# Kernel tuning notes

Hardware: AMD Instinct MI355X
Metric: run time of the kernel (lower is better)

Reference implementation:

```python
import jax, jax.numpy as jnp
import numpy as np

N_NODES = 50000
N_EDGES = 800000
N_GRAPHS = 128
ORIG_FEA = 92
NBR_FEA = 41
H = 64
N_CONV = 3
BN_EPS = 1e-5


def setup_inputs() -> dict:
    key = jax.random.key(0)
    ks = jax.random.split(key, 16)
    x = jax.random.normal(ks[0], (N_NODES, ORIG_FEA), dtype=jnp.float32)
    edge_attr = jax.random.normal(ks[1], (N_EDGES, NBR_FEA), dtype=jnp.float32)
    edge_index = jax.random.randint(ks[2], (2, N_EDGES), 0, N_NODES)
    batch = jnp.sort(jax.random.randint(ks[3], (N_NODES,), 0, N_GRAPHS))
    s_emb1 = 1.0 / np.sqrt(ORIG_FEA)
    s_emb2 = 1.0 / np.sqrt(NBR_FEA)
    s_conv = 1.0 / np.sqrt(3 * H)
    s_h = 1.0 / np.sqrt(H)
    return {
        "x": x,
        "edge_attr": edge_attr,
        "edge_index": edge_index,
        "batch": batch,
        "W_emb1": jax.random.uniform(ks[4], (ORIG_FEA, H), jnp.float32, -s_emb1, s_emb1),
        "b_emb1": jnp.zeros((H,), jnp.float32),
        "W_emb2": jax.random.uniform(ks[5], (NBR_FEA, H), jnp.float32, -s_emb2, s_emb2),
        "b_emb2": jnp.zeros((H,), jnp.float32),
        "Wf": jax.random.uniform(ks[6], (N_CONV, 3 * H, H), jnp.float32, -s_conv, s_conv),
        "bf": jnp.zeros((N_CONV, H), jnp.float32),
        "Ws": jax.random.uniform(ks[7], (N_CONV, 3 * H, H), jnp.float32, -s_conv, s_conv),
        "bs": jnp.zeros((N_CONV, H), jnp.float32),
        "gamma": jnp.ones((N_CONV, H), jnp.float32),
        "beta": jnp.zeros((N_CONV, H), jnp.float32),
        "W1": jax.random.uniform(ks[8], (H, H), jnp.float32, -s_h, s_h),
        "b1": jnp.zeros((H,), jnp.float32),
        "W2": jax.random.uniform(ks[9], (H, H), jnp.float32, -s_h, s_h),
        "b2": jnp.zeros((H,), jnp.float32),
        "Wo": jax.random.uniform(ks[10], (H, 1), jnp.float32, -s_h, s_h),
        "bo": jnp.zeros((1,), jnp.float32),
    }


def _batch_norm(h, g, b):
    # training-mode BatchNorm1d: biased batch statistics
    mu = jnp.mean(h, axis=0)
    var = jnp.var(h, axis=0)
    return (h - mu) * jax.lax.rsqrt(var + BN_EPS) * g + b


def reference(x, edge_attr, edge_index, batch, W_emb1, b_emb1, W_emb2, b_emb2,
              Wf, bf, Ws, bs, gamma, beta, W1, b1, W2, b2, Wo, bo):
    src = edge_index[0]  # x_j (source)
    dst = edge_index[1]  # x_i (target, aggregation index)
    h = x @ W_emb1 + b_emb1              # [N, H]
    e = edge_attr @ W_emb2 + b_emb2      # [E, H]
    for a in range(N_CONV):
        # CGConv: z_ij = [x_i, x_j, e_ij]; msg = sigmoid(lin_f(z)) * softplus(lin_s(z))
        z = jnp.concatenate([h[dst], h[src], e], axis=1)       # [E, 3H]
        msg = jax.nn.sigmoid(z @ Wf[a] + bf[a]) * jax.nn.softplus(z @ Ws[a] + bs[a])
        h = h + jax.ops.segment_sum(msg, dst, num_segments=N_NODES)
        h = _batch_norm(h, gamma[a], beta[a])
        if a != N_CONV - 1:
            h = jax.nn.relu(h)
        # dropout ratio is 0 -> no-op
    # JK='last' -> node representation is final h; mean pooling per graph
    sums = jax.ops.segment_sum(h, batch, num_segments=N_GRAPHS)              # [G, H]
    cnts = jax.ops.segment_sum(jnp.ones((N_NODES,), h.dtype), batch, num_segments=N_GRAPHS)
    y = sums / jnp.maximum(cnts, 1.0)[:, None]
    y = jax.nn.softplus(y @ W1 + b1)
    y = jax.nn.softplus(y @ W2 + b2)
    y = (y @ Wo + bo).squeeze(-1)  # [G]
    return y
```

## Files before the change

kernel.cpp:

```cpp
#include <hip/hip_runtime.h>
#include <hip/hip_bf16.h>
#include <hip/hip_fp16.h>
#include <math.h>

#define N_NODES 50000
#define N_EDGES 800000
#define N_GRAPHS 128
#define ORIG_FEA 92
#define NBR_FEA 41
#define H 64
#define N_CONV 3
#define BN_EPS 1e-5f
#define KP 48

typedef _Float16 h8 __attribute__((ext_vector_type(8)));
typedef float f32x4 __attribute__((ext_vector_type(4)));

__device__ __forceinline__ float sigmoidf_(float x) {
    return __fdividef(1.f, 1.f + __expf(-x));
}
__device__ __forceinline__ float softplusf_(float x) {
    return fmaxf(x, 0.f) + __logf(1.f + __expf(-fabsf(x)));
}

__global__ __launch_bounds__(256) void fold_kernel(
    const float* __restrict__ W_emb2, const float* __restrict__ b_emb2,
    const float* __restrict__ Wf, const float* __restrict__ bf,
    const float* __restrict__ Ws, const float* __restrict__ bs,
    _Float16* __restrict__ W2frag, float* __restrict__ cfs) {
    int a = blockIdx.x >> 1, gate = blockIdx.x & 1;
    const float* W = (gate ? Ws : Wf) + a * 192 * H + 128 * H;
    const float* bias = (gate ? bs : bf) + a * H;
    _Float16* out = W2frag + a * 128 * 64;
    float* cout = cfs + a * 128;
    for (int idx = threadIdx.x; idx < 64 * 64; idx += blockDim.x) {
        int j = idx >> 6, k = idx & 63;
        float acc = 0.f;
        if (k < NBR_FEA)
            for (int m = 0; m < H; ++m) acc += W_emb2[k * H + m] * W[m * H + j];
        int frag = (gate * 4 + (j >> 4)) * 2 + (k >> 5);
        int lane = (((k & 31) >> 3) << 4) + (j & 15);
        out[(frag * 64 + lane) * 8 + (k & 7)] = (_Float16)acc;
    }
    for (int j = threadIdx.x; j < H; j += blockDim.x) {
        float acc = bias[j];
        for (int m = 0; m < H; ++m) acc += b_emb2[m] * W[m * H + j];
        cout[(j & 15) * 8 + gate * 4 + (j >> 4)] = acc;
    }
}

__global__ __launch_bounds__(256) void embed_kernel(
    const float* __restrict__ x, const float* __restrict__ W,
    const float* __restrict__ b, float* __restrict__ state) {
    __shared__ float lw[ORIG_FEA * H];
    for (int i = threadIdx.x; i < ORIG_FEA * H; i += blockDim.x) lw[i] = W[i];
    __syncthreads();
    int lane = threadIdx.x & 63;
    int wid = (blockIdx.x * blockDim.x + threadIdx.x) >> 6;
    int nw = (gridDim.x * blockDim.x) >> 6;
    for (int n = wid; n < N_NODES; n += nw) {
        int nu = __builtin_amdgcn_readfirstlane(n);
        const float* xr = x + (size_t)nu * ORIG_FEA;
        float acc = b[lane];
#pragma unroll
        for (int k = 0; k < ORIG_FEA; ++k) acc += xr[k] * lw[k * H + lane];
        state[(size_t)nu * H + lane] = acc;
    }
}

__global__ __launch_bounds__(256) void hist_kernel(
    const int* __restrict__ ei, int* __restrict__ deg) {
    int e = blockIdx.x * blockDim.x + threadIdx.x;
    if (e < N_EDGES) atomicAdd(&deg[ei[N_EDGES + e]], 1);
}

__global__ __launch_bounds__(256) void scan_kernel(
    const int* __restrict__ deg, int* __restrict__ off, int* __restrict__ cur) {
    __shared__ int part[256];
    const int CHN = (N_NODES + 255) / 256;
    int t = threadIdx.x;
    int lo = t * CHN, hi = min(lo + CHN, N_NODES);
    int s = 0;
    for (int i = lo; i < hi; ++i) s += deg[i];
    part[t] = s;
    __syncthreads();
    for (int o = 1; o < 256; o <<= 1) {
        int v = (t >= o) ? part[t - o] : 0;
        __syncthreads();
        part[t] += v;
        __syncthreads();
    }
    int run = (t == 0) ? 0 : part[t - 1];
    for (int i = lo; i < hi; ++i) {
        off[i] = run;
        cur[i] = run;
        run += deg[i];
    }
    if (t == 255) off[N_NODES] = run;
}

__global__ __launch_bounds__(256) void scatter_kernel(
    const int* __restrict__ ei, int* __restrict__ cur, int* __restrict__ pos,
    int* __restrict__ src_s) {
    int e = blockIdx.x * blockDim.x + threadIdx.x;
    if (e < N_EDGES) {
        int d = ei[N_EDGES + e];
        int p = atomicAdd(&cur[d], 1);
        pos[e] = p;
        src_s[p] = ei[e];
    }
}

__global__ __launch_bounds__(256) void pack_ea_kernel(
    const int* __restrict__ pos, const float* __restrict__ ea,
    _Float16* __restrict__ ea_p) {
    int lane = threadIdx.x & 63;
    int wid = (blockIdx.x * blockDim.x + threadIdx.x) >> 6;
    int nw = (gridDim.x * blockDim.x) >> 6;
    for (int e = wid; e < N_EDGES; e += nw) {
        int eu = __builtin_amdgcn_readfirstlane(e);
        int p = __builtin_amdgcn_readfirstlane(pos[eu]);
        unsigned dw = 0;
        if (lane < 21) {
            const float* er = ea + (size_t)eu * NBR_FEA;
            float v0 = er[2 * lane];
            float v1 = (2 * lane + 1 < NBR_FEA) ? er[2 * lane + 1] : 0.f;
            union { _Float16 h[2]; unsigned u; } cv;
            cv.h[0] = (_Float16)v0;
            cv.h[1] = (_Float16)v1;
            dw = cv.u;
        }
        if (lane < KP / 2)
            *(unsigned*)(ea_p + (size_t)p * KP + 2 * lane) = dw;
    }
}

__global__ __launch_bounds__(256) void node_proj_bn_kernel(
    const float* __restrict__ state, const float* __restrict__ stats,
    const float* __restrict__ gamma, const float* __restrict__ beta,
    const float* __restrict__ Wf, const float* __restrict__ Ws,
    float* __restrict__ NPi, float* __restrict__ NPj, int mode) {
    __shared__ float lw[4 * H * H];
    __shared__ float slot[4][H];
    for (int i = threadIdx.x; i < H * H; i += blockDim.x) {
        lw[i] = Wf[i];
        lw[H * H + i] = Wf[H * H + i];
        lw[2 * H * H + i] = Ws[i];
        lw[3 * H * H + i] = Ws[H * H + i];
    }
    int lane = threadIdx.x & 63;
    int wl = threadIdx.x >> 6;
    int gbase = (lane & 15) * 8 + (lane >> 4);
    float A = 1.f, B = 0.f;
    if (mode) {
        const float inv_n = 1.f / (float)N_NODES;
        float mu = stats[lane] * inv_n;
        float var = stats[H + lane] * inv_n - mu * mu;
        float inv = rsqrtf(var + BN_EPS);
        A = inv * gamma[lane];
        B = beta[lane] - mu * A;
    }
    __syncthreads();
    int wid = (blockIdx.x * blockDim.x + threadIdx.x) >> 6;
    int nw = (gridDim.x * blockDim.x) >> 6;
    for (int n = wid; n < N_NODES; n += nw) {
        float z = state[(size_t)n * H + lane];
        float hn = mode ? fmaxf(z * A + B, 0.f) : z;
        slot[wl][lane] = hn;
        float pf = 0.f, qf = 0.f, ps = 0.f, qs = 0.f;
#pragma unroll
        for (int k = 0; k < H; ++k) {
            float s = slot[wl][k];
            pf += s * lw[k * H + lane];
            qf += s * lw[H * H + k * H + lane];
            ps += s * lw[2 * H * H + k * H + lane];
            qs += s * lw[3 * H * H + k * H + lane];
        }
        NPi[(size_t)n * 128 + gbase] = pf;
        NPi[(size_t)n * 128 + gbase + 4] = ps;
        NPj[(size_t)n * 128 + gbase] = qf;
        NPj[(size_t)n * 128 + gbase + 4] = qs;
    }
}

__global__ __launch_bounds__(256) void edge_mfma_kernel(
    const int* __restrict__ off, const int* __restrict__ src_s,
    const _Float16* __restrict__ ea_p,
    const float* __restrict__ NPi, const float* __restrict__ NPj,
    const _Float16* __restrict__ W2frag, const float* __restrict__ cfs,
    const float* __restrict__ stats_prev, const float* __restrict__ gamma,
    const float* __restrict__ beta, float* __restrict__ state,
    float* __restrict__ stats_out, int mode) {
    int lane = threadIdx.x & 63;
    int m15 = lane & 15, g = lane >> 4;
    h8 bfr[8][2];
#pragma unroll
    for (int nt = 0; nt < 8; ++nt)
#pragma unroll
        for (int ks = 0; ks < 2; ++ks) {
            union { uint4 u; h8 h; } cv;
            cv.u = *(const uint4*)(W2frag + (size_t)(((nt * 2 + ks) * 64) + lane) * 8);
            bfr[nt][ks] = cv.h;
        }
    f32x4 cflo = *(const f32x4*)(cfs + m15 * 8);
    f32x4 cfhi = *(const f32x4*)(cfs + m15 * 8 + 4);
    float A = 1.f, B = 0.f;
    if (mode) {
        const float inv_n = 1.f / (float)N_NODES;
        float mu = stats_prev[lane] * inv_n;
        float var = stats_prev[H + lane] * inv_n - mu * mu;
        float inv = rsqrtf(var + BN_EPS);
        A = inv * gamma[lane];
        B = beta[lane] - mu * A;
    }
    float s = 0.f, s2 = 0.f;
    int wid = (blockIdx.x * blockDim.x + threadIdx.x) >> 6;
    int nw = (gridDim.x * blockDim.x) >> 6;
    for (int n = wid; n < N_NODES; n += nw) {
        int nu = __builtin_amdgcn_readfirstlane(n);
        float z = state[(size_t)nu * H + lane];
        float acc = mode ? fmaxf(z * A + B, 0.f) : z;
        f32x4 nplo = *(const f32x4*)(NPi + (size_t)nu * 128 + m15 * 8);
        f32x4 nphi = *(const f32x4*)(NPi + (size_t)nu * 128 + m15 * 8 + 4);
        f32x4 bfv = cflo + nplo;
        f32x4 bsv = cfhi + nphi;
        int e0 = __builtin_amdgcn_readfirstlane(off[nu]);
        int e1 = __builtin_amdgcn_readfirstlane(off[nu + 1]);
        if (e0 >= e1) {
            state[(size_t)nu * H + lane] = acc;
            s += acc;
            s2 += acc * acc;
            continue;
        }
        h8 afr0, afr1;
        {
            int arow = min(e0 + m15, e1 - 1);
            const _Float16* rowp = ea_p + (size_t)arow * KP;
            union { uint4 u; h8 h; } cv0, cv1;
            cv0.u = *(const uint4*)(rowp + g * 8);
            afr0 = cv0.h;
            const _Float16* p1 = rowp + ((g < 2) ? (32 + g * 8) : 0);
            uint4 r1 = *(const uint4*)p1;
            if (g >= 2) { r1.x = 0u; r1.y = 0u; r1.z = 0u; r1.w = 0u; }
            cv1.u = r1;
            afr1 = cv1.h;
        }
        for (int e = e0; e < e1; e += 16) {
            int cnt = e1 - e;
            f32x4 c[8];
#pragma unroll
            for (int nt = 0; nt < 8; ++nt) c[nt] = (f32x4)(0.f);
#pragma unroll
            for (int nt = 0; nt < 8; ++nt)
                c[nt] = __builtin_amdgcn_mfma_f32_16x16x32_f16(afr0, bfr[nt][0],
                                                               c[nt], 0, 0, 0);
#pragma unroll
            for (int nt = 0; nt < 8; ++nt)
                c[nt] = __builtin_amdgcn_mfma_f32_16x16x32_f16(afr1, bfr[nt][1],
                                                               c[nt], 0, 0, 0);
            int en = e + 16;
            if (en < e1) {
                int arow = min(en + m15, e1 - 1);
                const _Float16* rowp = ea_p + (size_t)arow * KP;
                union { uint4 u; h8 h; } cv0, cv1;
                cv0.u = *(const uint4*)(rowp + g * 8);
                afr0 = cv0.h;
                const _Float16* p1 = rowp + ((g < 2) ? (32 + g * 8) : 0);
                uint4 r1 = *(const uint4*)p1;
                if (g >= 2) { r1.x = 0u; r1.y = 0u; r1.z = 0u; r1.w = 0u; }
                cv1.u = r1;
                afr1 = cv1.h;
            }
            f32x4 ql[4], qh[4];
            float mul[4];
#pragma unroll
            for (int r = 0; r < 4; ++r) {
                int rr = 4 * g + r;
                int ee = e + ((rr < cnt) ? rr : (cnt - 1));
                int sv = src_s[ee];
                const float* qp = NPj + (size_t)sv * 128 + m15 * 8;
                ql[r] = *(const f32x4*)qp;
                qh[r] = *(const f32x4*)(qp + 4);
                mul[r] = (rr < cnt) ? 1.f : 0.f;
            }
            float ts0 = 0.f, ts1 = 0.f, ts2 = 0.f, ts3 = 0.f;
#pragma unroll
            for (int r = 0; r < 4; ++r) {
                {
                    float af = c[0][r] + bfv[0] + ql[r][0];
                    float as = c[4][r] + bsv[0] + qh[r][0];
                    ts0 += mul[r] * sigmoidf_(af) * softplusf_(as);
                }
                {
                    float af = c[1][r] + bfv[1] + ql[r][1];
                    float as = c[5][r] + bsv[1] + qh[r][1];
                    ts1 += mul[r] * sigmoidf_(af) * softplusf_(as);
                }
                {
                    float af = c[2][r] + bfv[2] + ql[r][2];
                    float as = c[6][r] + bsv[2] + qh[r][2];
                    ts2 += mul[r] * sigmoidf_(af) * softplusf_(as);
                }
                {
                    float af = c[3][r] + bfv[3] + ql[r][3];
                    float as = c[7][r] + bsv[3] + qh[r][3];
                    ts3 += mul[r] * sigmoidf_(af) * softplusf_(as);
                }
            }
            ts0 += __shfl_xor(ts0, 16, 64); ts0 += __shfl_xor(ts0, 32, 64);
            ts1 += __shfl_xor(ts1, 16, 64); ts1 += __shfl_xor(ts1, 32, 64);
            ts2 += __shfl_xor(ts2, 16, 64); ts2 += __shfl_xor(ts2, 32, 64);
            ts3 += __shfl_xor(ts3, 16, 64); ts3 += __shfl_xor(ts3, 32, 64);
            float v = (g & 2) ? ((g & 1) ? ts3 : ts2) : ((g & 1) ? ts1 : ts0);
            acc += v;
        }
        state[(size_t)nu * H + lane] = acc;
        s += acc;
        s2 += acc * acc;
    }
    atomicAdd(&stats_out[lane], s);
    atomicAdd(&stats_out[H + lane], s2);
}

__global__ __launch_bounds__(256) void pool_bn_kernel(
    const float* __restrict__ state, const float* __restrict__ stats,
    const float* __restrict__ gamma, const float* __restrict__ beta,
    const int* __restrict__ batch, float* __restrict__ gsum,
    float* __restrict__ gcnt) {
    int lane = threadIdx.x & 63;
    const float inv_n = 1.f / (float)N_NODES;
    float mu = stats[lane] * inv_n;
    float var = stats[H + lane] * inv_n - mu * mu;
    float inv = rsqrtf(var + BN_EPS);
    float A = inv * gamma[lane];
    float B = beta[lane] - mu * A;
    int wid = (blockIdx.x * blockDim.x + threadIdx.x) >> 6;
    int nw = (gridDim.x * blockDim.x) >> 6;
    int per = (N_NODES + nw - 1) / nw;
    int lo = wid * per, hi = min(lo + per, N_NODES);
    if (lo >= hi) return;
    int gcur = __builtin_amdgcn_readfirstlane(batch[lo]);
    float accv = 0.f, cntv = 0.f;
    for (int n = lo; n < hi; ++n) {
        int gn = __builtin_amdgcn_readfirstlane(batch[n]);
        if (gn != gcur) {
            atomicAdd(&gsum[(size_t)gcur * H + lane], accv);
            if (lane == 0) atomicAdd(&gcnt[gcur], cntv);
            gcur = gn;
            accv = 0.f;
            cntv = 0.f;
        }
        accv += state[(size_t)n * H + lane] * A + B;
        cntv += 1.f;
    }
    atomicAdd(&gsum[(size_t)gcur * H + lane], accv);
    if (lane == 0) atomicAdd(&gcnt[gcur], cntv);
}

__global__ __launch_bounds__(64) void mlp_kernel(
    const float* __restrict__ gsum, const float* __restrict__ gcnt,
    const float* __restrict__ W1, const float* __restrict__ b1,
    const float* __restrict__ W2, const float* __restrict__ b2,
    const float* __restrict__ Wo, const float* __restrict__ bo,
    float* __restrict__ out) {
    int g = blockIdx.x;
    int lane = threadIdx.x;
    __shared__ float y[H];
    float cnt = fmaxf(gcnt[g], 1.f);
    y[lane] = gsum[(size_t)g * H + lane] / cnt;
    __syncthreads();
    float acc = b1[lane];
#pragma unroll
    for (int k = 0; k < H; ++k) acc += y[k] * W1[k * H + lane];
    float y1 = softplusf_(acc);
    __syncthreads();
    y[lane] = y1;
    __syncthreads();
    acc = b2[lane];
#pragma unroll
    for (int k = 0; k < H; ++k) acc += y[k] * W2[k * H + lane];
    float y2 = softplusf_(acc);
    float t = y2 * Wo[lane];
#pragma unroll
    for (int o = 32; o > 0; o >>= 1) t += __shfl_down(t, o, 64);
    if (lane == 0) out[g] = t + bo[0];
}

extern "C" void kernel_launch(void* const* d_in, const int* in_sizes, int n_in,
                              void* d_out, int out_size, void* d_ws, size_t ws_size,
                              hipStream_t stream) {
    const float* x = (const float*)d_in[0];
    const float* ea = (const float*)d_in[1];
    const int* ei = (const int*)d_in[2];
    const int* batch = (const int*)d_in[3];
    const float* W_emb1 = (const float*)d_in[4];
    const float* b_emb1 = (const float*)d_in[5];
    const float* W_emb2 = (const float*)d_in[6];
    const float* b_emb2 = (const float*)d_in[7];
    const float* Wf = (const float*)d_in[8];
    const float* bf = (const float*)d_in[9];
    const float* Ws = (const float*)d_in[10];
    const float* bs = (const float*)d_in[11];
    const float* gamma = (const float*)d_in[12];
    const float* beta = (const float*)d_in[13];
    const float* W1 = (const float*)d_in[14];
    const float* b1 = (const float*)d_in[15];
    const float* W2 = (const float*)d_in[16];
    const float* b2 = (const float*)d_in[17];
    const float* Wo = (const float*)d_in[18];
    const float* bo = (const float*)d_in[19];
    float* out = (float*)d_out;

    float* w = (float*)d_ws;
    float* stats = w;
    float* gsum = stats + 3 * 2 * H;
    float* gcnt = gsum + N_GRAPHS * H;
    int* deg = (int*)(gcnt + N_GRAPHS);
    const size_t zero_elems = 3 * 2 * H + N_GRAPHS * H + N_GRAPHS + N_NODES;
    _Float16* ea_p = (_Float16*)(w + zero_elems);
    int* off = (int*)(ea_p + (size_t)(N_EDGES + 8) * KP);
    int* cur = off + 50004;
    int* pos = cur + N_NODES;
    int* src_s = pos + N_EDGES;
    _Float16* W2frag = (_Float16*)(src_s + N_EDGES);
    float* cfs = (float*)(W2frag + 3 * 128 * 64);
    float* state = cfs + 3 * 128;
    float* NPi = state + (size_t)N_NODES * H;
    float* NPj = NPi + (size_t)N_NODES * 128;

    hipMemsetAsync(w, 0, zero_elems * sizeof(float), stream);

    fold_kernel<<<6, 256, 0, stream>>>(W_emb2, b_emb2, Wf, bf, Ws, bs, W2frag, cfs);
    embed_kernel<<<512, 256, 0, stream>>>(x, W_emb1, b_emb1, state);
    hist_kernel<<<(N_EDGES + 255) / 256, 256, 0, stream>>>(ei, deg);
    scan_kernel<<<1, 256, 0, stream>>>(deg, off, cur);
    scatter_kernel<<<(N_EDGES + 255) / 256, 256, 0, stream>>>(ei, cur, pos, src_s);
    pack_ea_kernel<<<2048, 256, 0, stream>>>(pos, ea, ea_p);

    for (int a = 0; a < N_CONV; ++a) {
        const float* sp = a > 0 ? stats + (a - 1) * 2 * H : stats;
        const float* gp = a > 0 ? gamma + (a - 1) * H : gamma;
        const float* bp = a > 0 ? beta + (a - 1) * H : beta;
        int mode = a > 0 ? 1 : 0;
        node_proj_bn_kernel<<<512, 256, 0, stream>>>(
            state, sp, gp, bp, Wf + a * 192 * H, Ws + a * 192 * H, NPi, NPj, mode);
        edge_mfma_kernel<<<2048, 256, 0, stream>>>(
            off, src_s, ea_p, NPi, NPj, W2frag + a * 128 * 64, cfs + a * 128,
            sp, gp, bp, state, stats + a * 2 * H, mode);
    }

    pool_bn_kernel<<<784, 256, 0, stream>>>(state, stats + 2 * 2 * H,
                                            gamma + 2 * H, beta + 2 * H,
                                            batch, gsum, gcnt);
    mlp_kernel<<<128, 64, 0, stream>>>(gsum, gcnt, W1, b1, W2, b2, Wo, bo, out);
}
```

Measured before the change: 1.248 ms.

## Use MFMA for node projections, store source projections in fp16, move edge weights to LDS

The scalar FMA node projection is replaced by an fp16 MFMA kernel that uses pre-packed concatenated Wf/Ws fragments, prepared by a new prep kernel. The source-side projection NPj is stored as fp16, which halves the bytes of the per-edge random gather. The edge kernel now reads its weight fragments from shared memory instead of holding them in registers, to cut register pressure and raise occupancy. It also drops the software prefetch of the next edge tile and changes the grid size. Risks are fp16 rounding error on the projected features and extra LDS traffic in the edge loop.

```diff
diff --git a/kernel.cpp b/kernel.cpp
--- a/kernel.cpp
+++ b/kernel.cpp
@@ -49,6 +49,23 @@
     }
 }
 
+__global__ __launch_bounds__(256) void prep_wcat_kernel(
+    const float* __restrict__ Wf, const float* __restrict__ Ws,
+    _Float16* __restrict__ Wcat_frag) {
+    int a = blockIdx.x;
+    _Float16* out = Wcat_frag + a * 64 * 256;
+    for (int idx = threadIdx.x; idx < 64 * 256; idx += blockDim.x) {
+        int k = idx >> 8, col = idx & 255;
+        int proj = col >> 6, j = col & 63;
+        int gate = proj & 1, ij = proj >> 1;
+        const float* W = (gate ? Ws : Wf) + a * 192 * H;
+        float v = W[(ij * 64 + k) * H + j];
+        int nt = col >> 4;
+        int lane = (((k & 31) >> 3) << 4) + (j & 15);
+        out[((nt * 2 + (k >> 5)) * 64 + lane) * 8 + (k & 7)] = (_Float16)v;
+    }
+}
+
 __global__ __launch_bounds__(256) void embed_kernel(
     const float* __restrict__ x, const float* __restrict__ W,
     const float* __restrict__ b, float* __restrict__ state) {
@@ -135,73 +152,108 @@
     }
 }
 
-__global__ __launch_bounds__(256) void node_proj_bn_kernel(
+__global__ __launch_bounds__(256, 4) void node_proj_mfma_kernel(
     const float* __restrict__ state, const float* __restrict__ stats,
     const float* __restrict__ gamma, const float* __restrict__ beta,
-    const float* __restrict__ Wf, const float* __restrict__ Ws,
-    float* __restrict__ NPi, float* __restrict__ NPj, int mode) {
-    __shared__ float lw[4 * H * H];
-    __shared__ float slot[4][H];
-    for (int i = threadIdx.x; i < H * H; i += blockDim.x) {
-        lw[i] = Wf[i];
-        lw[H * H + i] = Wf[H * H + i];
-        lw[2 * H * H + i] = Ws[i];
-        lw[3 * H * H + i] = Ws[H * H + i];
-    }
+    const _Float16* __restrict__ Wcat_frag,
+    float* __restrict__ NPi, _Float16* __restrict__ NPj, int mode) {
+    __shared__ __align__(16) _Float16 lB[32 * 64 * 8];
+    for (int i = threadIdx.x * 8; i < 32 * 64 * 8; i += blockDim.x * 8)
+        *(uint4*)(lB + i) = *(const uint4*)(Wcat_frag + i);
+    __syncthreads();
     int lane = threadIdx.x & 63;
-    int wl = threadIdx.x >> 6;
-    int gbase = (lane & 15) * 8 + (lane >> 4);
-    float A = 1.f, B = 0.f;
-    if (mode) {
-        const float inv_n = 1.f / (float)N_NODES;
-        float mu = stats[lane] * inv_n;
-        float var = stats[H + lane] * inv_n - mu * mu;
-        float inv = rsqrtf(var + BN_EPS);
-        A = inv * gamma[lane];
-        B = beta[lane] - mu * A;
-    }
-    __syncthreads();
+    int m15 = lane & 15, g = lane >> 4;
+    f32x4 Ac[2][2], Bc[2][2];
+#pragma unroll
+    for (int ks = 0; ks < 2; ++ks)
+#pragma unroll
+        for (int hlf = 0; hlf < 2; ++hlf) {
+            int k0 = ks * 32 + g * 8 + hlf * 4;
+            if (mode) {
+                const float inv_n = 1.f / (float)N_NODES;
+                f32x4 sm = *(const f32x4*)(stats + k0);
+                f32x4 sq = *(const f32x4*)(stats + H + k0);
+                f32x4 gm = *(const f32x4*)(gamma + k0);
+                f32x4 bt = *(const f32x4*)(beta + k0);
+#pragma unroll
+                for (int i = 0; i < 4; ++i) {
+                    float mu = sm[i] * inv_n;
+                    float var = sq[i] * inv_n - mu * mu;
+                    float inv = rsqrtf(var + BN_EPS);
+                    Ac[ks][hlf][i] = inv * gm[i];
+                    Bc[ks][hlf][i] = bt[i] - mu * inv * gm[i];
+                }
+            } else {
+                Ac[ks][hlf] = (f32x4)(1.f);
+                Bc[ks][hlf] = (f32x4)(0.f);
+            }
+        }
     int wid = (blockIdx.x * blockDim.x + threadIdx.x) >> 6;
     int nw = (gridDim.x * blockDim.x) >> 6;
-    for (int n = wid; n < N_NODES; n += nw) {
-        float z = state[(size_t)n * H + lane];
-        float hn = mode ? fmaxf(z * A + B, 0.f) : z;
-        slot[wl][lane] = hn;
-        float pf = 0.f, qf = 0.f, ps = 0.f, qs = 0.f;
-#pragma unroll
-        for (int k = 0; k < H; ++k) {
-            float s = slot[wl][k];
-            pf += s * lw[k * H + lane];
-            qf += s * lw[H * H + k * H + lane];
-            ps += s * lw[2 * H * H + k * H + lane];
-            qs += s * lw[3 * H * H + k * H + lane];
-        }
-        NPi[(size_t)n * 128 + gbase] = pf;
-        NPi[(size_t)n * 128 + gbase + 4] = ps;
-        NPj[(size_t)n * 128 + gbase] = qf;
-        NPj[(size_t)n * 128 + gbase + 4] = qs;
-    }
-}
-
-__global__ __launch_bounds__(256) void edge_mfma_kernel(
+    for (int t = wid; t < 3125; t += nw) {
+        int node = t * 16 + m15;
+        const float* sr = state + (size_t)node * H;
+        h8 afr[2];
+#pragma unroll
+        for (int ks = 0; ks < 2; ++ks) {
+            f32x4 z0 = *(const f32x4*)(sr + ks * 32 + g * 8);
+            f32x4 z1 = *(const f32x4*)(sr + ks * 32 + g * 8 + 4);
+            h8 a;
+#pragma unroll
+            for (int i = 0; i < 4; ++i) {
+                float v0 = z0[i] * Ac[ks][0][i] + Bc[ks][0][i];
+                float v1 = z1[i] * Ac[ks][1][i] + Bc[ks][1][i];
+                if (mode) { v0 = fmaxf(v0, 0.f); v1 = fmaxf(v1, 0.f); }
+                a[i] = (_Float16)v0;
+                a[4 + i] = (_Float16)v1;
+            }
+            afr[ks] = a;
+        }
+        f32x4 c[16];
+#pragma unroll
+        for (int nt = 0; nt < 16; ++nt) c[nt] = (f32x4)(0.f);
+#pragma unroll
+        for (int ks = 0; ks < 2; ++ks)
+#pragma unroll
+            for (int nt = 0; nt < 16; ++nt) {
+                h8 b = *(const h8*)(lB + ((size_t)(nt * 2 + ks) * 64 + lane) * 8);
+                c[nt] = __builtin_amdgcn_mfma_f32_16x16x32_f16(afr[ks], b, c[nt],
+                                                               0, 0, 0);
+            }
+#pragma unroll
+        for (int r = 0; r < 4; ++r) {
+            int nr = t * 16 + 4 * g + r;
+            f32x4 lo, hi;
+            h8 qj;
+#pragma unroll
+            for (int fq = 0; fq < 4; ++fq) {
+                lo[fq] = c[fq][r];
+                hi[fq] = c[4 + fq][r];
+                qj[fq] = (_Float16)c[8 + fq][r];
+                qj[4 + fq] = (_Float16)c[12 + fq][r];
+            }
+            float* pi = NPi + (size_t)nr * 128 + m15 * 8;
+            *(f32x4*)pi = lo;
+            *(f32x4*)(pi + 4) = hi;
+            *(h8*)(NPj + (size_t)nr * 128 + m15 * 8) = qj;
+        }
+    }
+}
+
+__global__ __launch_bounds__(256, 5) void edge_mfma_kernel(
     const int* __restrict__ off, const int* __restrict__ src_s,
     const _Float16* __restrict__ ea_p,
-    const float* __restrict__ NPi, const float* __restrict__ NPj,
+    const float* __restrict__ NPi, const _Float16* __restrict__ NPj,
     const _Float16* __restrict__ W2frag, const float* __restrict__ cfs,
     const float* __restrict__ stats_prev, const float* __restrict__ gamma,
     const float* __restrict__ beta, float* __restrict__ state,
     float* __restrict__ stats_out, int mode) {
+    __shared__ __align__(16) _Float16 lB[128 * 64];
+    for (int i = threadIdx.x * 8; i < 128 * 64; i += blockDim.x * 8)
+        *(uint4*)(lB + i) = *(const uint4*)(W2frag + i);
+    __syncthreads();
     int lane = threadIdx.x & 63;
     int m15 = lane & 15, g = lane >> 4;
-    h8 bfr[8][2];
-#pragma unroll
-    for (int nt = 0; nt < 8; ++nt)
-#pragma unroll
-        for (int ks = 0; ks < 2; ++ks) {
-            union { uint4 u; h8 h; } cv;
-            cv.u = *(const uint4*)(W2frag + (size_t)(((nt * 2 + ks) * 64) + lane) * 8);
-            bfr[nt][ks] = cv.h;
-        }
     f32x4 cflo = *(const f32x4*)(cfs + m15 * 8);
     f32x4 cfhi = *(const f32x4*)(cfs + m15 * 8 + 4);
     float A = 1.f, B = 0.f;
@@ -226,42 +278,12 @@
         f32x4 bsv = cfhi + nphi;
         int e0 = __builtin_amdgcn_readfirstlane(off[nu]);
         int e1 = __builtin_amdgcn_readfirstlane(off[nu + 1]);
-        if (e0 >= e1) {
-            state[(size_t)nu * H + lane] = acc;
-            s += acc;
-            s2 += acc * acc;
-            continue;
-        }
-        h8 afr0, afr1;
-        {
-            int arow = min(e0 + m15, e1 - 1);
-            const _Float16* rowp = ea_p + (size_t)arow * KP;
-            union { uint4 u; h8 h; } cv0, cv1;
-            cv0.u = *(const uint4*)(rowp + g * 8);
-            afr0 = cv0.h;
-            const _Float16* p1 = rowp + ((g < 2) ? (32 + g * 8) : 0);
-            uint4 r1 = *(const uint4*)p1;
-            if (g >= 2) { r1.x = 0u; r1.y = 0u; r1.z = 0u; r1.w = 0u; }
-            cv1.u = r1;
-            afr1 = cv1.h;
-        }
         for (int e = e0; e < e1; e += 16) {
             int cnt = e1 - e;
-            f32x4 c[8];
-#pragma unroll
-            for (int nt = 0; nt < 8; ++nt) c[nt] = (f32x4)(0.f);
-#pragma unroll
-            for (int nt = 0; nt < 8; ++nt)
-                c[nt] = __builtin_amdgcn_mfma_f32_16x16x32_f16(afr0, bfr[nt][0],
-                                                               c[nt], 0, 0, 0);
-#pragma unroll
-            for (int nt = 0; nt < 8; ++nt)
-                c[nt] = __builtin_amdgcn_mfma_f32_16x16x32_f16(afr1, bfr[nt][1],
-                                                               c[nt], 0, 0, 0);
-            int en = e + 16;
-            if (en < e1) {
-                int arow = min(en + m15, e1 - 1);
-                const _Float16* rowp = ea_p + (size_t)arow * KP;
+            int arow = e + (m15 < cnt ? m15 : 0);
+            const _Float16* rowp = ea_p + (size_t)arow * KP;
+            h8 afr0, afr1;
+            {
                 union { uint4 u; h8 h; } cv0, cv1;
                 cv0.u = *(const uint4*)(rowp + g * 8);
                 afr0 = cv0.h;
@@ -271,39 +293,52 @@
                 cv1.u = r1;
                 afr1 = cv1.h;
             }
-            f32x4 ql[4], qh[4];
+            h8 ql[4];
             float mul[4];
 #pragma unroll
             for (int r = 0; r < 4; ++r) {
                 int rr = 4 * g + r;
                 int ee = e + ((rr < cnt) ? rr : (cnt - 1));
                 int sv = src_s[ee];
-                const float* qp = NPj + (size_t)sv * 128 + m15 * 8;
-                ql[r] = *(const f32x4*)qp;
-                qh[r] = *(const f32x4*)(qp + 4);
+                ql[r] = *(const h8*)(NPj + (size_t)sv * 128 + m15 * 8);
                 mul[r] = (rr < cnt) ? 1.f : 0.f;
+            }
+            f32x4 c[8];
+#pragma unroll
+            for (int nt = 0; nt < 8; ++nt) c[nt] = (f32x4)(0.f);
+#pragma unroll
+            for (int nt = 0; nt < 8; ++nt) {
+                h8 b = *(const h8*)(lB + ((size_t)(nt * 2) * 64 + lane) * 8);
+                c[nt] = __builtin_amdgcn_mfma_f32_16x16x32_f16(afr0, b, c[nt],
+                                                               0, 0, 0);
+            }
+#pragma unroll
+            for (int nt = 0; nt < 8; ++nt) {
+                h8 b = *(const h8*)(lB + ((size_t)(nt * 2 + 1) * 64 + lane) * 8);
+                c[nt] = __builtin_amdgcn_mfma_f32_16x16x32_f16(afr1, b, c[nt],
+                                                               0, 0, 0);
             }
             float ts0 = 0.f, ts1 = 0.f, ts2 = 0.f, ts3 = 0.f;
 #pragma unroll
             for (int r = 0; r < 4; ++r) {
                 {
-                    float af = c[0][r] + bfv[0] + ql[r][0];
-                    float as = c[4][r] + bsv[0] + qh[r][0];
+                    float af = c[0][r] + bfv[0] + (float)ql[r][0];
+                    float as = c[4][r] + bsv[0] + (float)ql[r][4];
                     ts0 += mul[r] * sigmoidf_(af) * softplusf_(as);
                 }
                 {
-                    float af = c[1][r] + bfv[1] + ql[r][1];
-                    float as = c[5][r] + bsv[1] + qh[r][1];
+                    float af = c[1][r] + bfv[1] + (float)ql[r][1];
+                    float as = c[5][r] + bsv[1] + (float)ql[r][5];
                     ts1 += mul[r] * sigmoidf_(af) * softplusf_(as);
                 }
                 {
-                    float af = c[2][r] + bfv[2] + ql[r][2];
-                    float as = c[6][r] + bsv[2] + qh[r][2];
+                    float af = c[2][r] + bfv[2] + (float)ql[r][2];
+                    float as = c[6][r] + bsv[2] + (float)ql[r][6];
                     ts2 += mul[r] * sigmoidf_(af) * softplusf_(as);
                 }
                 {
-                    float af = c[3][r] + bfv[3] + ql[r][3];
-                    float as = c[7][r] + bsv[3] + qh[r][3];
+                    float af = c[3][r] + bfv[3] + (float)ql[r][3];
+                    float as = c[7][r] + bsv[3] + (float)ql[r][7];
                     ts3 += mul[r] * sigmoidf_(af) * softplusf_(as);
                 }
             }
@@ -423,14 +458,16 @@
     int* pos = cur + N_NODES;
     int* src_s = pos + N_EDGES;
     _Float16* W2frag = (_Float16*)(src_s + N_EDGES);
-    float* cfs = (float*)(W2frag + 3 * 128 * 64);
+    _Float16* Wcat_frag = W2frag + 3 * 128 * 64;
+    float* cfs = (float*)(Wcat_frag + 3 * 64 * 256);
     float* state = cfs + 3 * 128;
     float* NPi = state + (size_t)N_NODES * H;
-    float* NPj = NPi + (size_t)N_NODES * 128;
+    _Float16* NPj = (_Float16*)(NPi + (size_t)N_NODES * 128);
 
     hipMemsetAsync(w, 0, zero_elems * sizeof(float), stream);
 
     fold_kernel<<<6, 256, 0, stream>>>(W_emb2, b_emb2, Wf, bf, Ws, bs, W2frag, cfs);
+    prep_wcat_kernel<<<3, 256, 0, stream>>>(Wf, Ws, Wcat_frag);
     embed_kernel<<<512, 256, 0, stream>>>(x, W_emb1, b_emb1, state);
     hist_kernel<<<(N_EDGES + 255) / 256, 256, 0, stream>>>(ei, deg);
     scan_kernel<<<1, 256, 0, stream>>>(deg, off, cur);
@@ -442,9 +479,9 @@
         const float* gp = a > 0 ? gamma + (a - 1) * H : gamma;
         const float* bp = a > 0 ? beta + (a - 1) * H : beta;
         int mode = a > 0 ? 1 : 0;
-        node_proj_bn_kernel<<<512, 256, 0, stream>>>(
-            state, sp, gp, bp, Wf + a * 192 * H, Ws + a * 192 * H, NPi, NPj, mode);
-        edge_mfma_kernel<<<2048, 256, 0, stream>>>(
+        node_proj_mfma_kernel<<<512, 256, 0, stream>>>(
+            state, sp, gp, bp, Wcat_frag + a * 64 * 256, NPi, NPj, mode);
+        edge_mfma_kernel<<<1280, 256, 0, stream>>>(
             off, src_s, ea_p, NPi, NPj, W2frag + a * 128 * 64, cfs + a * 128,
             sp, gp, bp, state, stats + a * 2 * H, mode);
     }
```

New measurement: 1.819 ms. 1.46x slower.
